# Optimization experiments

Measured on AMD Instinct MI355X. Metric: run time of the kernel, lower is better.

The kernel has to match this reference:

```python
import jax, jax.numpy as jnp
import numpy as np

N_NODES = 100000
N_EDGES = 3200000
D_FEAT = 128
N_CLASSES = 8


def setup_inputs() -> dict:
    key = jax.random.key(0)
    ks = jax.random.split(key, 8)
    x = jax.random.normal(ks[0], (N_NODES, D_FEAT), dtype=jnp.float32)
    edge_index = jax.random.randint(ks[1], (2, N_EDGES), 0, N_NODES, dtype=jnp.int64)
    W1 = jax.random.normal(ks[2], (D_FEAT, 32), dtype=jnp.float32) / np.sqrt(D_FEAT)
    b1 = jnp.zeros((32,), dtype=jnp.float32)
    W2 = jax.random.normal(ks[3], (32, 16), dtype=jnp.float32) / np.sqrt(32)
    b2 = jnp.zeros((16,), dtype=jnp.float32)
    Wc = jax.random.normal(ks[4], (16, N_CLASSES), dtype=jnp.float32) / np.sqrt(16)
    bc = jnp.zeros((N_CLASSES,), dtype=jnp.float32)
    return {"x": x, "edge_index": edge_index, "W1": W1, "b1": b1,
            "W2": W2, "b2": b2, "Wc": Wc, "bc": bc}


def _gcn_conv(h, src, dst, norm, W, b, num_nodes):
    # PyG GCNConv: linear transform, then sym-normalized scatter-add, then bias
    h = h @ W                                   # [N, out]
    msg = h[src] * norm[:, None]                # [E+N, out] gather + scale
    out = jax.ops.segment_sum(msg, dst, num_segments=num_nodes)
    return out + b


def reference(x, edge_index, W1, b1, W2, b2, Wc, bc):
    num_nodes = x.shape[0]
    loop = jnp.arange(num_nodes, dtype=edge_index.dtype)
    src = jnp.concatenate([edge_index[0], loop])  # add self-loops (PyG default)
    dst = jnp.concatenate([edge_index[1], loop])
    deg = jax.ops.segment_sum(jnp.ones_like(dst, dtype=x.dtype), dst,
                              num_segments=num_nodes)
    dinv = jnp.where(deg > 0, jax.lax.rsqrt(deg), 0.0)
    norm = dinv[src] * dinv[dst]                # symmetric normalization per edge

    h = _gcn_conv(x, src, dst, norm, W1, b1, num_nodes)
    h = jax.nn.relu(h)
    # dropout p=0.5 is identity in eval mode (training=False)
    h = _gcn_conv(h, src, dst, norm, W2, b2, num_nodes)
    h = jax.nn.relu(h)
    logits = h @ Wc + bc
    return jax.nn.log_softmax(logits, axis=1)
```

## Files before the change

kernel.cpp:

```cpp
#include <hip/hip_runtime.h>
#include <math.h>

#define N_NODES 100000
#define N_EDGES 3200000
#define D_FEAT 128
#define H1 32
#define H2 16
#define NC 8

#define NBUCK 391
#define BCAP 16384
#define EPB 4096
#define EPT 8

typedef short s16x8 __attribute__((ext_vector_type(8)));
typedef float f32x4 __attribute__((ext_vector_type(4)));

__device__ inline unsigned short f2bf(float f) {
    unsigned int u = __float_as_uint(f);
    u += 0x7FFF + ((u >> 16) & 1);
    return (unsigned short)(u >> 16);
}
__device__ inline float bf2f(unsigned short h) {
    return __uint_as_float((unsigned int)h << 16);
}


__global__ void k_detect(const int* __restrict__ ei, const float* __restrict__ W1,
                         int* __restrict__ meta, int* __restrict__ bucket_cursor,
                         unsigned short* __restrict__ W1f) {
    __shared__ int red[256];
    int v = 0;
    for (int i = threadIdx.x; i < 1024; i += 256) v |= ei[2 * i + 1];
    red[threadIdx.x] = v;
    __syncthreads();
    for (int s = 128; s > 0; s >>= 1) {
        if (threadIdx.x < (unsigned)s) red[threadIdx.x] |= red[threadIdx.x + s];
        __syncthreads();
    }
    if (threadIdx.x == 0) meta[0] = (red[0] == 0) ? 1 : 0;
    for (int i = threadIdx.x; i < NBUCK; i += 256) bucket_cursor[i] = 0;
    for (int idx = threadIdx.x; idx < 2 * 4 * 64 * 8; idx += 256) {
        const int j    = idx & 7;
        const int lane = (idx >> 3) & 63;
        const int kk   = (idx >> 9) & 3;
        const int nt   = idx >> 11;
        const int k = kk * 32 + ((lane >> 4) << 3) + j;
        const int n = nt * 16 + (lane & 15);
        W1f[idx] = f2bf(W1[k * H1 + n]);
    }
}


__global__ __launch_bounds__(512) void k_bscatter(const int* __restrict__ ei,
                                                  const int* __restrict__ meta,
                                                  int* __restrict__ bucket_cursor,
                                                  int* __restrict__ ebuf) {
    __shared__ int hist[NBUCK];
    __shared__ int lofs[NBUCK];
    __shared__ int rank[NBUCK];
    __shared__ int gb[NBUCK];
    __shared__ int sc[512];
    __shared__ int pay[EPB];
    __shared__ unsigned short pbk[EPB];
    const int tid = threadIdx.x;
    for (int i = tid; i < NBUCK; i += 512) { hist[i] = 0; rank[i] = 0; }
    __syncthreads();
    const int e0 = blockIdx.x * EPB;
    const int n = min(EPB, N_EDGES - e0);
    const bool is64 = (meta[0] != 0);
    int rs[EPT], rd[EPT];
    if (is64) {
#pragma unroll
        for (int k = 0; k < EPT / 2; ++k) {
            const int i = 2 * (tid + k * 512);
            if (i < n) {
                const int e = e0 + i;
                const int4 s = *(const int4*)&ei[2 * e];
                const int4 d = *(const int4*)&ei[2 * N_EDGES + 2 * e];
                rs[2 * k] = s.x; rs[2 * k + 1] = s.z;
                rd[2 * k] = d.x; rd[2 * k + 1] = d.z;
                atomicAdd(&hist[d.x >> 8], 1);
                atomicAdd(&hist[d.z >> 8], 1);
            }
        }
    } else {
#pragma unroll
        for (int k = 0; k < EPT / 2; ++k) {
            const int i = 2 * (tid + k * 512);
            if (i < n) {
                const int e = e0 + i;
                const int2 s = *(const int2*)&ei[e];
                const int2 d = *(const int2*)&ei[N_EDGES + e];
                rs[2 * k] = s.x; rs[2 * k + 1] = s.y;
                rd[2 * k] = d.x; rd[2 * k + 1] = d.y;
                atomicAdd(&hist[d.x >> 8], 1);
                atomicAdd(&hist[d.y >> 8], 1);
            }
        }
    }
    __syncthreads();
    const int own = (tid < NBUCK) ? hist[tid] : 0;
    sc[tid] = own;
    __syncthreads();
    for (int off = 1; off < 512; off <<= 1) {
        const int v = (tid >= off) ? sc[tid - off] : 0;
        __syncthreads();
        sc[tid] += v;
        __syncthreads();
    }
    if (tid < NBUCK) {
        lofs[tid] = sc[tid] - own;
        if (own > 0) gb[tid] = tid * BCAP + atomicAdd(&bucket_cursor[tid], own);
    }
    __syncthreads();
#pragma unroll
    for (int k = 0; k < EPT / 2; ++k) {
        const int i = 2 * (tid + k * 512);
        if (i < n) {
#pragma unroll
            for (int j = 0; j < 2; ++j) {
                const int b = rd[2 * k + j] >> 8;
                const int p = lofs[b] + atomicAdd(&rank[b], 1);
                pay[p] = (rs[2 * k + j] << 8) | (rd[2 * k + j] & 255);
                pbk[p] = (unsigned short)b;
            }
        }
    }
    __syncthreads();
    for (int p = tid; p < n; p += 512) {
        const int b = pbk[p];
        ebuf[gb[b] + (p - lofs[b])] = pay[p];
    }
}


__global__ __launch_bounds__(512) void k_bfill2(const int* __restrict__ ebuf,
                                                const int* __restrict__ bucket_cursor,
                                                int* __restrict__ row_ptr,
                                                float* __restrict__ dinv,
                                                int* __restrict__ col_idx) {
    __shared__ int h[512];
    __shared__ int cnt[256];
    __shared__ int sc[256];
    __shared__ int cur[256];
    __shared__ int srt[BCAP];
    __shared__ int s_wb, s_nb;
    const int b = blockIdx.x;
    const int tid = threadIdx.x;
    const int own0 = (tid < NBUCK) ? bucket_cursor[tid] : 0;
    h[tid] = own0;
    if (tid < 256) cnt[tid] = 0;
    __syncthreads();
    for (int off = 1; off < 512; off <<= 1) {
        const int v = (tid >= off) ? h[tid - off] : 0;
        __syncthreads();
        h[tid] += v;
        __syncthreads();
    }
    if (tid == b) { s_wb = h[tid] - own0; s_nb = own0; }
    __syncthreads();
    const int wb = s_wb;
    const int nb = s_nb;
    const int rb = b * BCAP;
    for (int i = tid; i < nb; i += 512)
        atomicAdd(&cnt[ebuf[rb + i] & 255], 1);
    __syncthreads();
    int own = 0;
    if (tid < 256) { own = cnt[tid]; sc[tid] = own; }
    __syncthreads();
    for (int off = 1; off < 256; off <<= 1) {
        const int v = (tid < 256 && tid >= off) ? sc[tid - off] : 0;
        __syncthreads();
        if (tid < 256) sc[tid] += v;
        __syncthreads();
    }
    if (tid < 256) {
        const int excl = sc[tid] - own;
        const int v = (b << 8) + tid;
        if (v <= N_NODES) row_ptr[v] = wb + excl;
        if (v < N_NODES) dinv[v] = rsqrtf(1.0f + (float)own);
        cur[tid] = excl;
    }
    __syncthreads();
    for (int i = tid; i < nb; i += 512) {
        const int pk = ebuf[rb + i];
        const int slot = atomicAdd(&cur[pk & 255], 1);
        srt[slot] = pk >> 8;
    }
    __syncthreads();
    for (int i = tid; i < nb; i += 512)
        col_idx[wb + i] = srt[i];
}


__global__ __launch_bounds__(256) void k_gemm1m(const float* __restrict__ x,
                                                const unsigned short* __restrict__ W1f,
                                                const float* __restrict__ dinv,
                                                unsigned int* __restrict__ u1q) {
    __shared__ float os[4][16][33];
    const int tid = threadIdx.x;
    const int w = tid >> 6;
    const int lane = tid & 63;
    const int row0 = (blockIdx.x * 4 + w) * 16;
    const bool act = (row0 < N_NODES);
    if (act) {
        const int m = lane & 15;
        const int quad = lane >> 4;
        const s16x8* bf = (const s16x8*)W1f;
        f32x4 acc0 = {0.f, 0.f, 0.f, 0.f};
        f32x4 acc1 = {0.f, 0.f, 0.f, 0.f};
#pragma unroll
        for (int kk = 0; kk < 4; ++kk) {
            const float* xp = x + (size_t)(row0 + m) * D_FEAT + kk * 32 + quad * 8;
            const float4 p0 = ((const float4*)xp)[0];
            const float4 p1 = ((const float4*)xp)[1];
            s16x8 a;
            a[0] = (short)f2bf(p0.x); a[1] = (short)f2bf(p0.y);
            a[2] = (short)f2bf(p0.z); a[3] = (short)f2bf(p0.w);
            a[4] = (short)f2bf(p1.x); a[5] = (short)f2bf(p1.y);
            a[6] = (short)f2bf(p1.z); a[7] = (short)f2bf(p1.w);
            acc0 = __builtin_amdgcn_mfma_f32_16x16x32_bf16(a, bf[kk * 64 + lane], acc0, 0, 0, 0);
            acc1 = __builtin_amdgcn_mfma_f32_16x16x32_bf16(a, bf[(4 + kk) * 64 + lane], acc1, 0, 0, 0);
        }
#pragma unroll
        for (int r = 0; r < 4; ++r) {
            os[w][quad * 4 + r][m]      = acc0[r];
            os[w][quad * 4 + r][16 + m] = acc1[r];
        }
    }
    __syncthreads();
    if (act) {
        const int rl = lane >> 2;
        const int seg = lane & 3;
        const int row = row0 + rl;
        const float dv = dinv[row];
        const float* p = &os[w][rl][seg * 8];
        unsigned int pk0 = __builtin_amdgcn_cvt_pk_fp8_f32(p[0] * dv, p[1] * dv, 0u, false);
        pk0 = __builtin_amdgcn_cvt_pk_fp8_f32(p[2] * dv, p[3] * dv, pk0, true);
        unsigned int pk1 = __builtin_amdgcn_cvt_pk_fp8_f32(p[4] * dv, p[5] * dv, 0u, false);
        pk1 = __builtin_amdgcn_cvt_pk_fp8_f32(p[6] * dv, p[7] * dv, pk1, true);
        uint2 o; o.x = pk0; o.y = pk1;
        ((uint2*)u1q)[(size_t)row * 4 + seg] = o;
    }
}


#define ACC8(Q) do { \
    a0 += __builtin_amdgcn_cvt_f32_fp8((Q).x, 0); \
    a1 += __builtin_amdgcn_cvt_f32_fp8((Q).x, 1); \
    a2 += __builtin_amdgcn_cvt_f32_fp8((Q).x, 2); \
    a3 += __builtin_amdgcn_cvt_f32_fp8((Q).x, 3); \
    a4 += __builtin_amdgcn_cvt_f32_fp8((Q).y, 0); \
    a5 += __builtin_amdgcn_cvt_f32_fp8((Q).y, 1); \
    a6 += __builtin_amdgcn_cvt_f32_fp8((Q).y, 2); \
    a7 += __builtin_amdgcn_cvt_f32_fp8((Q).y, 3); \
} while (0)

__global__ __launch_bounds__(256) void k_pull1f(const int* __restrict__ row_ptr,
                                                const int* __restrict__ col_idx,
                                                const float* __restrict__ dinv,
                                                const unsigned int* __restrict__ u1q,
                                                const float* __restrict__ b1,
                                                const float* __restrict__ W2,
                                                unsigned int* __restrict__ u2b) {
    __shared__ float Ws[H1 * H2];
    __shared__ float hs[64][33];
    const int tid = threadIdx.x;
    for (int i = tid; i < H1 * H2; i += 256) Ws[i] = W2[i];
    const int n = tid >> 2;
    const int lq = tid & 3;
    const int lb = (tid & 63) & ~3;
    const int v = blockIdx.x * 64 + n;
    float dv = 0.0f;
    if (v < N_NODES) {
        const uint2* base = (const uint2*)u1q;
        uint2 q = base[(size_t)v * 4 + lq];
        float a0 = __builtin_amdgcn_cvt_f32_fp8(q.x, 0);
        float a1 = __builtin_amdgcn_cvt_f32_fp8(q.x, 1);
        float a2 = __builtin_amdgcn_cvt_f32_fp8(q.x, 2);
        float a3 = __builtin_amdgcn_cvt_f32_fp8(q.x, 3);
        float a4 = __builtin_amdgcn_cvt_f32_fp8(q.y, 0);
        float a5 = __builtin_amdgcn_cvt_f32_fp8(q.y, 1);
        float a6 = __builtin_amdgcn_cvt_f32_fp8(q.y, 2);
        float a7 = __builtin_amdgcn_cvt_f32_fp8(q.y, 3);
        const int beg = row_ptr[v];
        const int end = row_ptr[v + 1];
        int i = beg;
        for (; i + 8 <= end; i += 8) {
            const int c0 = col_idx[i + lq];
            const int c1 = col_idx[i + 4 + lq];
            const int s0 = __shfl(c0, lb + 0, 64);
            const int s1 = __shfl(c0, lb + 1, 64);
            const int s2 = __shfl(c0, lb + 2, 64);
            const int s3 = __shfl(c0, lb + 3, 64);
            const int s4 = __shfl(c1, lb + 0, 64);
            const int s5 = __shfl(c1, lb + 1, 64);
            const int s6 = __shfl(c1, lb + 2, 64);
            const int s7 = __shfl(c1, lb + 3, 64);
            const uint2 q0 = base[(size_t)s0 * 4 + lq];
            const uint2 q1 = base[(size_t)s1 * 4 + lq];
            const uint2 q2 = base[(size_t)s2 * 4 + lq];
            const uint2 q3 = base[(size_t)s3 * 4 + lq];
            const uint2 q4 = base[(size_t)s4 * 4 + lq];
            const uint2 q5 = base[(size_t)s5 * 4 + lq];
            const uint2 q6 = base[(size_t)s6 * 4 + lq];
            const uint2 q7 = base[(size_t)s7 * 4 + lq];
            ACC8(q0); ACC8(q1); ACC8(q2); ACC8(q3);
            ACC8(q4); ACC8(q5); ACC8(q6); ACC8(q7);
        }
        for (; i + 4 <= end; i += 4) {
            const int c0 = col_idx[i + lq];
            const int s0 = __shfl(c0, lb + 0, 64);
            const int s1 = __shfl(c0, lb + 1, 64);
            const int s2 = __shfl(c0, lb + 2, 64);
            const int s3 = __shfl(c0, lb + 3, 64);
            const uint2 q0 = base[(size_t)s0 * 4 + lq];
            const uint2 q1 = base[(size_t)s1 * 4 + lq];
            const uint2 q2 = base[(size_t)s2 * 4 + lq];
            const uint2 q3 = base[(size_t)s3 * 4 + lq];
            ACC8(q0); ACC8(q1); ACC8(q2); ACC8(q3);
        }
        for (; i < end; ++i) {
            const int s = col_idx[i];
            const uint2 qq = base[(size_t)s * 4 + lq];
            ACC8(qq);
        }
        dv = dinv[v];
        const float4 bb0 = ((const float4*)b1)[lq * 2];
        const float4 bb1 = ((const float4*)b1)[lq * 2 + 1];
        float* hp = &hs[n][lq * 8];
        hp[0] = fmaxf(fmaf(a0, dv, bb0.x), 0.0f);
        hp[1] = fmaxf(fmaf(a1, dv, bb0.y), 0.0f);
        hp[2] = fmaxf(fmaf(a2, dv, bb0.z), 0.0f);
        hp[3] = fmaxf(fmaf(a3, dv, bb0.w), 0.0f);
        hp[4] = fmaxf(fmaf(a4, dv, bb1.x), 0.0f);
        hp[5] = fmaxf(fmaf(a5, dv, bb1.y), 0.0f);
        hp[6] = fmaxf(fmaf(a6, dv, bb1.z), 0.0f);
        hp[7] = fmaxf(fmaf(a7, dv, bb1.w), 0.0f);
    }
    __syncthreads();
    if (v < N_NODES) {
        const int j0 = lq * 4;
        float s0 = 0.f, s1 = 0.f, s2 = 0.f, s3 = 0.f;
#pragma unroll
        for (int k = 0; k < H1; ++k) {
            const float hk = hs[n][k];
            s0 = fmaf(hk, Ws[k * H2 + j0 + 0], s0);
            s1 = fmaf(hk, Ws[k * H2 + j0 + 1], s1);
            s2 = fmaf(hk, Ws[k * H2 + j0 + 2], s2);
            s3 = fmaf(hk, Ws[k * H2 + j0 + 3], s3);
        }
        uint2 o;
        o.x = (unsigned int)f2bf(s0 * dv) | ((unsigned int)f2bf(s1 * dv) << 16);
        o.y = (unsigned int)f2bf(s2 * dv) | ((unsigned int)f2bf(s3 * dv) << 16);
        ((uint2*)u2b)[(size_t)v * 4 + lq] = o;
    }
}


#define ACC4(Q) do { \
    a0 += bf2f((unsigned short)(Q).x); \
    a1 += bf2f((unsigned short)((Q).x >> 16)); \
    a2 += bf2f((unsigned short)(Q).y); \
    a3 += bf2f((unsigned short)((Q).y >> 16)); \
} while (0)

__global__ __launch_bounds__(256) void k_pull2f(const int* __restrict__ row_ptr,
                                                const int* __restrict__ col_idx,
                                                const float* __restrict__ dinv,
                                                const unsigned int* __restrict__ u2b,
                                                const float* __restrict__ b2,
                                                const float* __restrict__ Wc,
                                                const float* __restrict__ bc,
                                                float* __restrict__ out) {
    __shared__ float hs[64][17];
    __shared__ float Wcs[H2 * NC];
    __shared__ float bcs[NC];
    const int tid = threadIdx.x;
    if (tid < H2 * NC) Wcs[tid] = Wc[tid];
    if (tid < NC) bcs[tid] = bc[tid];
    const int n = tid >> 2;
    const int lq = tid & 3;
    const int lb = (tid & 63) & ~3;
    const int v = blockIdx.x * 64 + n;
    if (v < N_NODES) {
        const uint2* base = (const uint2*)u2b;
        uint2 q = base[(size_t)v * 4 + lq];
        float a0 = bf2f((unsigned short)q.x), a1 = bf2f((unsigned short)(q.x >> 16));
        float a2 = bf2f((unsigned short)q.y), a3 = bf2f((unsigned short)(q.y >> 16));
        const int beg = row_ptr[v];
        const int end = row_ptr[v + 1];
        int i = beg;
        for (; i + 8 <= end; i += 8) {
            const int c0 = col_idx[i + lq];
            const int c1 = col_idx[i + 4 + lq];
            const int s0 = __shfl(c0, lb + 0, 64);
            const int s1 = __shfl(c0, lb + 1, 64);
            const int s2 = __shfl(c0, lb + 2, 64);
            const int s3 = __shfl(c0, lb + 3, 64);
            const int s4 = __shfl(c1, lb + 0, 64);
            const int s5 = __shfl(c1, lb + 1, 64);
            const int s6 = __shfl(c1, lb + 2, 64);
            const int s7 = __shfl(c1, lb + 3, 64);
            const uint2 q0 = base[(size_t)s0 * 4 + lq];
            const uint2 q1 = base[(size_t)s1 * 4 + lq];
            const uint2 q2 = base[(size_t)s2 * 4 + lq];
            const uint2 q3 = base[(size_t)s3 * 4 + lq];
            const uint2 q4 = base[(size_t)s4 * 4 + lq];
            const uint2 q5 = base[(size_t)s5 * 4 + lq];
            const uint2 q6 = base[(size_t)s6 * 4 + lq];
            const uint2 q7 = base[(size_t)s7 * 4 + lq];
            ACC4(q0); ACC4(q1); ACC4(q2); ACC4(q3);
            ACC4(q4); ACC4(q5); ACC4(q6); ACC4(q7);
        }
        for (; i + 4 <= end; i += 4) {
            const int c0 = col_idx[i + lq];
            const int s0 = __shfl(c0, lb + 0, 64);
            const int s1 = __shfl(c0, lb + 1, 64);
            const int s2 = __shfl(c0, lb + 2, 64);
            const int s3 = __shfl(c0, lb + 3, 64);
            const uint2 q0 = base[(size_t)s0 * 4 + lq];
            const uint2 q1 = base[(size_t)s1 * 4 + lq];
            const uint2 q2 = base[(size_t)s2 * 4 + lq];
            const uint2 q3 = base[(size_t)s3 * 4 + lq];
            ACC4(q0); ACC4(q1); ACC4(q2); ACC4(q3);
        }
        for (; i < end; ++i) {
            const int s = col_idx[i];
            const uint2 qq = base[(size_t)s * 4 + lq];
            ACC4(qq);
        }
        const float dv = dinv[v];
        const float4 bb = ((const float4*)b2)[lq];
        float* hp = &hs[n][lq * 4];
        hp[0] = fmaxf(fmaf(a0, dv, bb.x), 0.0f);
        hp[1] = fmaxf(fmaf(a1, dv, bb.y), 0.0f);
        hp[2] = fmaxf(fmaf(a2, dv, bb.z), 0.0f);
        hp[3] = fmaxf(fmaf(a3, dv, bb.w), 0.0f);
    }
    __syncthreads();
    if (tid < 64) {
        const int vv = blockIdx.x * 64 + tid;
        if (vv < N_NODES) {
            float lg[NC];
#pragma unroll
            for (int j = 0; j < NC; ++j) lg[j] = bcs[j];
#pragma unroll
            for (int k = 0; k < H2; ++k) {
                const float hk = hs[tid][k];
#pragma unroll
                for (int j = 0; j < NC; ++j)
                    lg[j] = fmaf(hk, Wcs[k * NC + j], lg[j]);
            }
            float m = lg[0];
#pragma unroll
            for (int j = 1; j < NC; ++j) m = fmaxf(m, lg[j]);
            float s = 0.0f;
#pragma unroll
            for (int j = 0; j < NC; ++j) s += expf(lg[j] - m);
            const float lse = logf(s) + m;
            float4 o0, o1;
            o0.x = lg[0] - lse; o0.y = lg[1] - lse;
            o0.z = lg[2] - lse; o0.w = lg[3] - lse;
            o1.x = lg[4] - lse; o1.y = lg[5] - lse;
            o1.z = lg[6] - lse; o1.w = lg[7] - lse;
            float4* op = (float4*)(out + (size_t)vv * NC);
            op[0] = o0; op[1] = o1;
        }
    }
}


extern "C" void kernel_launch(void* const* d_in, const int* in_sizes, int n_in,
                              void* d_out, int out_size, void* d_ws, size_t ws_size,
                              hipStream_t stream) {
    const float* x   = (const float*)d_in[0];
    const int*   ei  = (const int*)d_in[1];
    const float* W1  = (const float*)d_in[2];
    const float* b1  = (const float*)d_in[3];
    const float* W2  = (const float*)d_in[4];
    const float* b2  = (const float*)d_in[5];
    const float* Wc  = (const float*)d_in[6];
    const float* bc  = (const float*)d_in[7];
    float* out = (float*)d_out;

    int*   meta          = (int*)d_ws;
    int*   bucket_cursor = meta + 16;
    int*   bucket_base   = bucket_cursor + 512;
    int*   row_ptr       = bucket_base + 512;
    float* dinv          = (float*)(row_ptr + 100016);
    unsigned short* W1f  = (unsigned short*)(dinv + 100000);
    int*   col_idx       = (int*)W1f + 2048;
    int*   ebuf          = col_idx + 3200000;
    unsigned int* u1q    = (unsigned int*)ebuf;
    unsigned int* u2b    = (unsigned int*)(ebuf + NBUCK * BCAP);

    k_detect  <<<1, 256, 0, stream>>>(ei, W1, meta, bucket_cursor, W1f);
    k_bscatter<<<(N_EDGES + EPB - 1) / EPB, 512, 0, stream>>>(ei, meta, bucket_cursor, ebuf);
    k_bfill2  <<<NBUCK, 512, 0, stream>>>(ebuf, bucket_cursor, row_ptr, dinv, col_idx);

    k_gemm1m<<<(N_NODES + 63) / 64, 256, 0, stream>>>(x, W1f, dinv, u1q);
    k_pull1f<<<(N_NODES + 63) / 64, 256, 0, stream>>>(row_ptr, col_idx, dinv, u1q, b1, W2, u2b);
    k_pull2f<<<(N_NODES + 63) / 64, 256, 0, stream>>>(row_ptr, col_idx, dinv, u2b, b2, Wc, bc, out);
}
```

Measured before the change: 209.8 us.

## Stage CSR neighbor indices in LDS and split each node's edges across two lane groups

The two pull kernels now handle 32 nodes per block. Each block first copies its contiguous col_idx range into shared memory, falling back to global reads when the range exceeds capacity. Each node's edges are split between two groups of 4 lanes that interleave over the edges, and a shuffle-xor reduction combines their partial sums, which doubles the number of concurrent gathers per node. The Hillis-Steele block scans in the bucket scatter and fill kernels are replaced by wave-shuffle scans that need fewer barriers. The costs are more blocks, extra LDS use that may reduce occupancy, and the assumption that N_NODES is divisible by 32 (there is no tail guard).

```diff
diff --git a/kernel.cpp b/kernel.cpp
--- a/kernel.cpp
+++ b/kernel.cpp
@@ -13,6 +13,9 @@
 #define EPB 4096
 #define EPT 8
 
+#define P_NODES 32
+#define P_CAP 3072
+
 typedef short s16x8 __attribute__((ext_vector_type(8)));
 typedef float f32x4 __attribute__((ext_vector_type(4)));
 
@@ -23,6 +26,15 @@
 }
 __device__ inline float bf2f(unsigned short h) {
     return __uint_as_float((unsigned int)h << 16);
+}
+
+__device__ inline int wave_scan_incl(int v, int lane) {
+#pragma unroll
+    for (int off = 1; off < 64; off <<= 1) {
+        const int t = __shfl_up(v, off, 64);
+        if (lane >= off) v += t;
+    }
+    return v;
 }
 
 
@@ -60,10 +72,12 @@
     __shared__ int lofs[NBUCK];
     __shared__ int rank[NBUCK];
     __shared__ int gb[NBUCK];
-    __shared__ int sc[512];
+    __shared__ int wsum[8];
     __shared__ int pay[EPB];
     __shared__ unsigned short pbk[EPB];
     const int tid = threadIdx.x;
+    const int lane = tid & 63;
+    const int wid = tid >> 6;
     for (int i = tid; i < NBUCK; i += 512) { hist[i] = 0; rank[i] = 0; }
     __syncthreads();
     const int e0 = blockIdx.x * EPB;
@@ -101,16 +115,18 @@
     }
     __syncthreads();
     const int own = (tid < NBUCK) ? hist[tid] : 0;
-    sc[tid] = own;
-    __syncthreads();
-    for (int off = 1; off < 512; off <<= 1) {
-        const int v = (tid >= off) ? sc[tid - off] : 0;
-        __syncthreads();
-        sc[tid] += v;
-        __syncthreads();
-    }
+    int incl = wave_scan_incl(own, lane);
+    if (lane == 63) wsum[wid] = incl;
+    __syncthreads();
+    if (tid == 0) {
+        int r = 0;
+#pragma unroll
+        for (int w = 0; w < 8; ++w) { const int t = wsum[w]; wsum[w] = r; r += t; }
+    }
+    __syncthreads();
+    incl += wsum[wid];
     if (tid < NBUCK) {
-        lofs[tid] = sc[tid] - own;
+        lofs[tid] = incl - own;
         if (own > 0) gb[tid] = tid * BCAP + atomicAdd(&bucket_cursor[tid], own);
     }
     __syncthreads();
@@ -140,25 +156,28 @@
                                                 int* __restrict__ row_ptr,
                                                 float* __restrict__ dinv,
                                                 int* __restrict__ col_idx) {
-    __shared__ int h[512];
     __shared__ int cnt[256];
-    __shared__ int sc[256];
     __shared__ int cur[256];
+    __shared__ int wsum[8];
     __shared__ int srt[BCAP];
     __shared__ int s_wb, s_nb;
     const int b = blockIdx.x;
     const int tid = threadIdx.x;
+    const int lane = tid & 63;
+    const int wid = tid >> 6;
     const int own0 = (tid < NBUCK) ? bucket_cursor[tid] : 0;
-    h[tid] = own0;
     if (tid < 256) cnt[tid] = 0;
-    __syncthreads();
-    for (int off = 1; off < 512; off <<= 1) {
-        const int v = (tid >= off) ? h[tid - off] : 0;
-        __syncthreads();
-        h[tid] += v;
-        __syncthreads();
-    }
-    if (tid == b) { s_wb = h[tid] - own0; s_nb = own0; }
+    int incl0 = wave_scan_incl(own0, lane);
+    if (lane == 63) wsum[wid] = incl0;
+    __syncthreads();
+    if (tid == 0) {
+        int r = 0;
+#pragma unroll
+        for (int w = 0; w < 8; ++w) { const int t = wsum[w]; wsum[w] = r; r += t; }
+    }
+    __syncthreads();
+    incl0 += wsum[wid];
+    if (tid == b) { s_wb = incl0 - own0; s_nb = own0; }
     __syncthreads();
     const int wb = s_wb;
     const int nb = s_nb;
@@ -166,17 +185,19 @@
     for (int i = tid; i < nb; i += 512)
         atomicAdd(&cnt[ebuf[rb + i] & 255], 1);
     __syncthreads();
-    int own = 0;
-    if (tid < 256) { own = cnt[tid]; sc[tid] = own; }
-    __syncthreads();
-    for (int off = 1; off < 256; off <<= 1) {
-        const int v = (tid < 256 && tid >= off) ? sc[tid - off] : 0;
-        __syncthreads();
-        if (tid < 256) sc[tid] += v;
-        __syncthreads();
-    }
+    const int own = (tid < 256) ? cnt[tid] : 0;
+    int incl = wave_scan_incl(own, lane);
+    if (lane == 63) wsum[wid] = incl;
+    __syncthreads();
+    if (tid == 0) {
+        int r = 0;
+#pragma unroll
+        for (int w = 0; w < 8; ++w) { const int t = wsum[w]; wsum[w] = r; r += t; }
+    }
+    __syncthreads();
+    incl += wsum[wid];
     if (tid < 256) {
-        const int excl = sc[tid] - own;
+        const int excl = incl - own;
         const int v = (b << 8) + tid;
         if (v <= N_NODES) row_ptr[v] = wb + excl;
         if (v < N_NODES) dinv[v] = rsqrtf(1.0f + (float)own);
@@ -265,39 +286,48 @@
                                                 const float* __restrict__ W2,
                                                 unsigned int* __restrict__ u2b) {
     __shared__ float Ws[H1 * H2];
-    __shared__ float hs[64][33];
+    __shared__ float hs[P_NODES][33];
+    __shared__ int lidx[P_CAP];
     const int tid = threadIdx.x;
     for (int i = tid; i < H1 * H2; i += 256) Ws[i] = W2[i];
-    const int n = tid >> 2;
+    const int v0 = blockIdx.x * P_NODES;
+    const int base_off = row_ptr[v0];
+    const int range = row_ptr[v0 + P_NODES] - base_off;
+    const bool ovf = (range > P_CAP);
+    const int stg = ovf ? 0 : range;
+    for (int j = tid; j < stg; j += 256) lidx[j] = col_idx[base_off + j];
+    __syncthreads();
+    const int n = tid >> 3;
+    const int half = (tid >> 2) & 1;
     const int lq = tid & 3;
-    const int lb = (tid & 63) & ~3;
-    const int v = blockIdx.x * 64 + n;
-    float dv = 0.0f;
-    if (v < N_NODES) {
-        const uint2* base = (const uint2*)u1q;
-        uint2 q = base[(size_t)v * 4 + lq];
-        float a0 = __builtin_amdgcn_cvt_f32_fp8(q.x, 0);
-        float a1 = __builtin_amdgcn_cvt_f32_fp8(q.x, 1);
-        float a2 = __builtin_amdgcn_cvt_f32_fp8(q.x, 2);
-        float a3 = __builtin_amdgcn_cvt_f32_fp8(q.x, 3);
-        float a4 = __builtin_amdgcn_cvt_f32_fp8(q.y, 0);
-        float a5 = __builtin_amdgcn_cvt_f32_fp8(q.y, 1);
-        float a6 = __builtin_amdgcn_cvt_f32_fp8(q.y, 2);
-        float a7 = __builtin_amdgcn_cvt_f32_fp8(q.y, 3);
-        const int beg = row_ptr[v];
-        const int end = row_ptr[v + 1];
-        int i = beg;
-        for (; i + 8 <= end; i += 8) {
-            const int c0 = col_idx[i + lq];
-            const int c1 = col_idx[i + 4 + lq];
-            const int s0 = __shfl(c0, lb + 0, 64);
-            const int s1 = __shfl(c0, lb + 1, 64);
-            const int s2 = __shfl(c0, lb + 2, 64);
-            const int s3 = __shfl(c0, lb + 3, 64);
-            const int s4 = __shfl(c1, lb + 0, 64);
-            const int s5 = __shfl(c1, lb + 1, 64);
-            const int s6 = __shfl(c1, lb + 2, 64);
-            const int s7 = __shfl(c1, lb + 3, 64);
+    const int v = v0 + n;
+    const uint2* base = (const uint2*)u1q;
+    float a0 = 0.f, a1 = 0.f, a2 = 0.f, a3 = 0.f;
+    float a4 = 0.f, a5 = 0.f, a6 = 0.f, a7 = 0.f;
+    if (half == 0) {
+        const uint2 q = base[(size_t)v * 4 + lq];
+        a0 = __builtin_amdgcn_cvt_f32_fp8(q.x, 0);
+        a1 = __builtin_amdgcn_cvt_f32_fp8(q.x, 1);
+        a2 = __builtin_amdgcn_cvt_f32_fp8(q.x, 2);
+        a3 = __builtin_amdgcn_cvt_f32_fp8(q.x, 3);
+        a4 = __builtin_amdgcn_cvt_f32_fp8(q.y, 0);
+        a5 = __builtin_amdgcn_cvt_f32_fp8(q.y, 1);
+        a6 = __builtin_amdgcn_cvt_f32_fp8(q.y, 2);
+        a7 = __builtin_amdgcn_cvt_f32_fp8(q.y, 3);
+    }
+    const int beg = row_ptr[v] - base_off;
+    const int end = row_ptr[v + 1] - base_off;
+    int i = beg + half;
+    if (!ovf) {
+        for (; i + 14 < end; i += 16) {
+            const int s0 = lidx[i];
+            const int s1 = lidx[i + 2];
+            const int s2 = lidx[i + 4];
+            const int s3 = lidx[i + 6];
+            const int s4 = lidx[i + 8];
+            const int s5 = lidx[i + 10];
+            const int s6 = lidx[i + 12];
+            const int s7 = lidx[i + 14];
             const uint2 q0 = base[(size_t)s0 * 4 + lq];
             const uint2 q1 = base[(size_t)s1 * 4 + lq];
             const uint2 q2 = base[(size_t)s2 * 4 + lq];
@@ -309,24 +339,54 @@
             ACC8(q0); ACC8(q1); ACC8(q2); ACC8(q3);
             ACC8(q4); ACC8(q5); ACC8(q6); ACC8(q7);
         }
-        for (; i + 4 <= end; i += 4) {
-            const int c0 = col_idx[i + lq];
-            const int s0 = __shfl(c0, lb + 0, 64);
-            const int s1 = __shfl(c0, lb + 1, 64);
-            const int s2 = __shfl(c0, lb + 2, 64);
-            const int s3 = __shfl(c0, lb + 3, 64);
+        for (; i + 6 < end; i += 8) {
+            const int s0 = lidx[i];
+            const int s1 = lidx[i + 2];
+            const int s2 = lidx[i + 4];
+            const int s3 = lidx[i + 6];
             const uint2 q0 = base[(size_t)s0 * 4 + lq];
             const uint2 q1 = base[(size_t)s1 * 4 + lq];
             const uint2 q2 = base[(size_t)s2 * 4 + lq];
             const uint2 q3 = base[(size_t)s3 * 4 + lq];
             ACC8(q0); ACC8(q1); ACC8(q2); ACC8(q3);
         }
-        for (; i < end; ++i) {
-            const int s = col_idx[i];
-            const uint2 qq = base[(size_t)s * 4 + lq];
+        for (; i < end; i += 2) {
+            const uint2 qq = base[(size_t)lidx[i] * 4 + lq];
             ACC8(qq);
         }
-        dv = dinv[v];
+    } else {
+        const int* gp = col_idx + base_off;
+        for (; i + 14 < end; i += 16) {
+            const int s0 = gp[i];
+            const int s1 = gp[i + 2];
+            const int s2 = gp[i + 4];
+            const int s3 = gp[i + 6];
+            const int s4 = gp[i + 8];
+            const int s5 = gp[i + 10];
+            const int s6 = gp[i + 12];
+            const int s7 = gp[i + 14];
+            const uint2 q0 = base[(size_t)s0 * 4 + lq];
+            const uint2 q1 = base[(size_t)s1 * 4 + lq];
+            const uint2 q2 = base[(size_t)s2 * 4 + lq];
+            const uint2 q3 = base[(size_t)s3 * 4 + lq];
+            const uint2 q4 = base[(size_t)s4 * 4 + lq];
+            const uint2 q5 = base[(size_t)s5 * 4 + lq];
+            const uint2 q6 = base[(size_t)s6 * 4 + lq];
+            const uint2 q7 = base[(size_t)s7 * 4 + lq];
+            ACC8(q0); ACC8(q1); ACC8(q2); ACC8(q3);
+            ACC8(q4); ACC8(q5); ACC8(q6); ACC8(q7);
+        }
+        for (; i < end; i += 2) {
+            const uint2 qq = base[(size_t)gp[i] * 4 + lq];
+            ACC8(qq);
+        }
+    }
+    a0 += __shfl_xor(a0, 4, 64); a1 += __shfl_xor(a1, 4, 64);
+    a2 += __shfl_xor(a2, 4, 64); a3 += __shfl_xor(a3, 4, 64);
+    a4 += __shfl_xor(a4, 4, 64); a5 += __shfl_xor(a5, 4, 64);
+    a6 += __shfl_xor(a6, 4, 64); a7 += __shfl_xor(a7, 4, 64);
+    if (half == 0) {
+        const float dv = dinv[v];
         const float4 bb0 = ((const float4*)b1)[lq * 2];
         const float4 bb1 = ((const float4*)b1)[lq * 2 + 1];
         float* hp = &hs[n][lq * 8];
@@ -338,14 +398,19 @@
         hp[5] = fmaxf(fmaf(a5, dv, bb1.y), 0.0f);
         hp[6] = fmaxf(fmaf(a6, dv, bb1.z), 0.0f);
         hp[7] = fmaxf(fmaf(a7, dv, bb1.w), 0.0f);
-    }
-    __syncthreads();
-    if (v < N_NODES) {
-        const int j0 = lq * 4;
+        if (lq == 0) hs[n][32] = dv;
+    }
+    __syncthreads();
+    if (tid < 4 * P_NODES) {
+        const int nn = tid >> 2;
+        const int jq = tid & 3;
+        const int vv = v0 + nn;
+        const int j0 = jq * 4;
+        const float dv = hs[nn][32];
         float s0 = 0.f, s1 = 0.f, s2 = 0.f, s3 = 0.f;
 #pragma unroll
         for (int k = 0; k < H1; ++k) {
-            const float hk = hs[n][k];
+            const float hk = hs[nn][k];
             s0 = fmaf(hk, Ws[k * H2 + j0 + 0], s0);
             s1 = fmaf(hk, Ws[k * H2 + j0 + 1], s1);
             s2 = fmaf(hk, Ws[k * H2 + j0 + 2], s2);
@@ -354,7 +419,7 @@
         uint2 o;
         o.x = (unsigned int)f2bf(s0 * dv) | ((unsigned int)f2bf(s1 * dv) << 16);
         o.y = (unsigned int)f2bf(s2 * dv) | ((unsigned int)f2bf(s3 * dv) << 16);
-        ((uint2*)u2b)[(size_t)v * 4 + lq] = o;
+        ((uint2*)u2b)[(size_t)vv * 4 + jq] = o;
     }
 }
 
@@ -374,35 +439,44 @@
                                                 const float* __restrict__ Wc,
                                                 const float* __restrict__ bc,
                                                 float* __restrict__ out) {
-    __shared__ float hs[64][17];
+    __shared__ float hs[P_NODES][17];
     __shared__ float Wcs[H2 * NC];
     __shared__ float bcs[NC];
+    __shared__ int lidx[P_CAP];
     const int tid = threadIdx.x;
     if (tid < H2 * NC) Wcs[tid] = Wc[tid];
     if (tid < NC) bcs[tid] = bc[tid];
-    const int n = tid >> 2;
+    const int v0 = blockIdx.x * P_NODES;
+    const int base_off = row_ptr[v0];
+    const int range = row_ptr[v0 + P_NODES] - base_off;
+    const bool ovf = (range > P_CAP);
+    const int stg = ovf ? 0 : range;
+    for (int j = tid; j < stg; j += 256) lidx[j] = col_idx[base_off + j];
+    __syncthreads();
+    const int n = tid >> 3;
+    const int half = (tid >> 2) & 1;
     const int lq = tid & 3;
-    const int lb = (tid & 63) & ~3;
-    const int v = blockIdx.x * 64 + n;
-    if (v < N_NODES) {
-        const uint2* base = (const uint2*)u2b;
-        uint2 q = base[(size_t)v * 4 + lq];
-        float a0 = bf2f((unsigned short)q.x), a1 = bf2f((unsigned short)(q.x >> 16));
-        float a2 = bf2f((unsigned short)q.y), a3 = bf2f((unsigned short)(q.y >> 16));
-        const int beg = row_ptr[v];
-        const int end = row_ptr[v + 1];
-        int i = beg;
-        for (; i + 8 <= end; i += 8) {
-            const int c0 = col_idx[i + lq];
-            const int c1 = col_idx[i + 4 + lq];
-            const int s0 = __shfl(c0, lb + 0, 64);
-            const int s1 = __shfl(c0, lb + 1, 64);
-            const int s2 = __shfl(c0, lb + 2, 64);
-            const int s3 = __shfl(c0, lb + 3, 64);
-            const int s4 = __shfl(c1, lb + 0, 64);
-            const int s5 = __shfl(c1, lb + 1, 64);
-            const int s6 = __shfl(c1, lb + 2, 64);
-            const int s7 = __shfl(c1, lb + 3, 64);
+    const int v = v0 + n;
+    const uint2* base = (const uint2*)u2b;
+    float a0 = 0.f, a1 = 0.f, a2 = 0.f, a3 = 0.f;
+    if (half == 0) {
+        const uint2 q = base[(size_t)v * 4 + lq];
+        a0 = bf2f((unsigned short)q.x); a1 = bf2f((unsigned short)(q.x >> 16));
+        a2 = bf2f((unsigned short)q.y); a3 = bf2f((unsigned short)(q.y >> 16));
+    }
+    const int beg = row_ptr[v] - base_off;
+    const int end = row_ptr[v + 1] - base_off;
+    int i = beg + half;
+    if (!ovf) {
+        for (; i + 14 < end; i += 16) {
+            const int s0 = lidx[i];
+            const int s1 = lidx[i + 2];
+            const int s2 = lidx[i + 4];
+            const int s3 = lidx[i + 6];
+            const int s4 = lidx[i + 8];
+            const int s5 = lidx[i + 10];
+            const int s6 = lidx[i + 12];
+            const int s7 = lidx[i + 14];
             const uint2 q0 = base[(size_t)s0 * 4 + lq];
             const uint2 q1 = base[(size_t)s1 * 4 + lq];
             const uint2 q2 = base[(size_t)s2 * 4 + lq];
@@ -414,23 +488,51 @@
             ACC4(q0); ACC4(q1); ACC4(q2); ACC4(q3);
             ACC4(q4); ACC4(q5); ACC4(q6); ACC4(q7);
         }
-        for (; i + 4 <= end; i += 4) {
-            const int c0 = col_idx[i + lq];
-            const int s0 = __shfl(c0, lb + 0, 64);
-            const int s1 = __shfl(c0, lb + 1, 64);
-            const int s2 = __shfl(c0, lb + 2, 64);
-            const int s3 = __shfl(c0, lb + 3, 64);
+        for (; i + 6 < end; i += 8) {
+            const int s0 = lidx[i];
+            const int s1 = lidx[i + 2];
+            const int s2 = lidx[i + 4];
+            const int s3 = lidx[i + 6];
             const uint2 q0 = base[(size_t)s0 * 4 + lq];
             const uint2 q1 = base[(size_t)s1 * 4 + lq];
             const uint2 q2 = base[(size_t)s2 * 4 + lq];
             const uint2 q3 = base[(size_t)s3 * 4 + lq];
             ACC4(q0); ACC4(q1); ACC4(q2); ACC4(q3);
         }
-        for (; i < end; ++i) {
-            const int s = col_idx[i];
-            const uint2 qq = base[(size_t)s * 4 + lq];
+        for (; i < end; i += 2) {
+            const uint2 qq = base[(size_t)lidx[i] * 4 + lq];
             ACC4(qq);
         }
+    } else {
+        const int* gp = col_idx + base_off;
+        for (; i + 14 < end; i += 16) {
+            const int s0 = gp[i];
+            const int s1 = gp[i + 2];
+            const int s2 = gp[i + 4];
+            const int s3 = gp[i + 6];
+            const int s4 = gp[i + 8];
+            const int s5 = gp[i + 10];
+            const int s6 = gp[i + 12];
+            const int s7 = gp[i + 14];
+            const uint2 q0 = base[(size_t)s0 * 4 + lq];
+            const uint2 q1 = base[(size_t)s1 * 4 + lq];
+            const uint2 q2 = base[(size_t)s2 * 4 + lq];
+            const uint2 q3 = base[(size_t)s3 * 4 + lq];
+            const uint2 q4 = base[(size_t)s4 * 4 + lq];
+            const uint2 q5 = base[(size_t)s5 * 4 + lq];
+            const uint2 q6 = base[(size_t)s6 * 4 + lq];
+            const uint2 q7 = base[(size_t)s7 * 4 + lq];
+            ACC4(q0); ACC4(q1); ACC4(q2); ACC4(q3);
+            ACC4(q4); ACC4(q5); ACC4(q6); ACC4(q7);
+        }
+        for (; i < end; i += 2) {
+            const uint2 qq = base[(size_t)gp[i] * 4 + lq];
+            ACC4(qq);
+        }
+    }
+    a0 += __shfl_xor(a0, 4, 64); a1 += __shfl_xor(a1, 4, 64);
+    a2 += __shfl_xor(a2, 4, 64); a3 += __shfl_xor(a3, 4, 64);
+    if (half == 0) {
         const float dv = dinv[v];
         const float4 bb = ((const float4*)b2)[lq];
         float* hp = &hs[n][lq * 4];
@@ -440,34 +542,32 @@
         hp[3] = fmaxf(fmaf(a3, dv, bb.w), 0.0f);
     }
     __syncthreads();
-    if (tid < 64) {
-        const int vv = blockIdx.x * 64 + tid;
-        if (vv < N_NODES) {
-            float lg[NC];
-#pragma unroll
-            for (int j = 0; j < NC; ++j) lg[j] = bcs[j];
-#pragma unroll
-            for (int k = 0; k < H2; ++k) {
-                const float hk = hs[tid][k];
-#pragma unroll
-                for (int j = 0; j < NC; ++j)
-                    lg[j] = fmaf(hk, Wcs[k * NC + j], lg[j]);
-            }
-            float m = lg[0];
-#pragma unroll
-            for (int j = 1; j < NC; ++j) m = fmaxf(m, lg[j]);
-            float s = 0.0f;
-#pragma unroll
-            for (int j = 0; j < NC; ++j) s += expf(lg[j] - m);
-            const float lse = logf(s) + m;
-            float4 o0, o1;
-            o0.x = lg[0] - lse; o0.y = lg[1] - lse;
-            o0.z = lg[2] - lse; o0.w = lg[3] - lse;
-            o1.x = lg[4] - lse; o1.y = lg[5] - lse;
-            o1.z = lg[6] - lse; o1.w = lg[7] - lse;
-            float4* op = (float4*)(out + (size_t)vv * NC);
-            op[0] = o0; op[1] = o1;
-        }
+    if (tid < P_NODES) {
+        const int vv = v0 + tid;
+        float lg[NC];
+#pragma unroll
+        for (int j = 0; j < NC; ++j) lg[j] = bcs[j];
+#pragma unroll
+        for (int k = 0; k < H2; ++k) {
+            const float hk = hs[tid][k];
+#pragma unroll
+            for (int j = 0; j < NC; ++j)
+                lg[j] = fmaf(hk, Wcs[k * NC + j], lg[j]);
+        }
+        float m = lg[0];
+#pragma unroll
+        for (int j = 1; j < NC; ++j) m = fmaxf(m, lg[j]);
+        float s = 0.0f;
+#pragma unroll
+        for (int j = 0; j < NC; ++j) s += expf(lg[j] - m);
+        const float lse = logf(s) + m;
+        float4 o0, o1;
+        o0.x = lg[0] - lse; o0.y = lg[1] - lse;
+        o0.z = lg[2] - lse; o0.w = lg[3] - lse;
+        o1.x = lg[4] - lse; o1.y = lg[5] - lse;
+        o1.z = lg[6] - lse; o1.w = lg[7] - lse;
+        float4* op = (float4*)(out + (size_t)vv * NC);
+        op[0] = o0; op[1] = o1;
     }
 }
 
@@ -501,6 +601,6 @@
     k_bfill2  <<<NBUCK, 512, 0, stream>>>(ebuf, bucket_cursor, row_ptr, dinv, col_idx);
 
     k_gemm1m<<<(N_NODES + 63) / 64, 256, 0, stream>>>(x, W1f, dinv, u1q);
-    k_pull1f<<<(N_NODES + 63) / 64, 256, 0, stream>>>(row_ptr, col_idx, dinv, u1q, b1, W2, u2b);
-    k_pull2f<<<(N_NODES + 63) / 64, 256, 0, stream>>>(row_ptr, col_idx, dinv, u2b, b2, Wc, bc, out);
-}
+    k_pull1f<<<N_NODES / P_NODES, 256, 0, stream>>>(row_ptr, col_idx, dinv, u1q, b1, W2, u2b);
+    k_pull2f<<<N_NODES / P_NODES, 256, 0, stream>>>(row_ptr, col_idx, dinv, u2b, b2, Wc, bc, out);
+}
```

New measurement: 200.0 us. -4.7%, faster.
